# Optimization experiments

Hardware: AMD Instinct MI355X
Metric: run time of the kernel (lower is better)

The kernel has to match this reference:

```python
import jax, jax.numpy as jnp
import numpy as np

MARGIN = 0.5


def _pairwise_dist(x):
    # Euclidean cdist via ||a||^2 + ||b||^2 - 2ab, with safe sqrt.
    sq = jnp.sum(x * x, axis=-1)  # (N,)
    d2 = sq[:, None] + sq[None, :] - 2.0 * (x @ x.T)
    d2 = jnp.maximum(d2, 0.0)
    return jnp.sqrt(jnp.where(d2 > 0.0, d2, 1.0)) * (d2 > 0.0)


def setup_inputs() -> dict:
    key = jax.random.key(0)
    k1, k2 = jax.random.split(key)
    N, D = 8192, 128
    embeddings = jax.random.normal(k1, (N, D), dtype=jnp.float32)
    labels = jax.random.randint(k2, (N,), 0, 7, dtype=jnp.int64)
    return {"embeddings": embeddings, "labels": labels}


def reference(embeddings, labels):
    N = embeddings.shape[0]
    dist = _pairwise_dist(embeddings)  # (N, N)
    same = labels[:, None] == labels[None, :]
    eye = jnp.eye(N, dtype=bool)
    pos_mask = same & ~eye
    neg_mask = ~same
    big = jnp.asarray(jnp.finfo(dist.dtype).max, dist.dtype)
    # hardest positive: max dist among same-label (excl. self)
    pos_dist = jnp.max(jnp.where(pos_mask, dist, -big), axis=1)
    # hardest negative: min dist among different-label
    neg_dist = jnp.min(jnp.where(neg_mask, dist, big), axis=1)
    valid = jnp.any(pos_mask, axis=1) & jnp.any(neg_mask, axis=1)
    per_row = jax.nn.relu(pos_dist - neg_dist + MARGIN)
    loss_sum = jnp.sum(jnp.where(valid, per_row, 0.0))
    count = jnp.sum(valid)
    return loss_sum / jnp.maximum(count, 1).astype(loss_sum.dtype)
```

## Files before the change

### kernel.cpp

```cpp
#include <hip/hip_runtime.h>

#define N 8192
#define D 128
#define MARGIN 0.5f
#define FLT_BIG 3.402823466e+38f

typedef __bf16 bf16x8 __attribute__((ext_vector_type(8)));
typedef float f32x4 __attribute__((ext_vector_type(4)));
typedef unsigned short u16x8 __attribute__((ext_vector_type(8)));

__device__ __forceinline__ unsigned short f2bf_rne(float f) {
  unsigned u = __float_as_uint(f);
  u += 0x7FFFu + ((u >> 16) & 1u);
  return (unsigned short)(u >> 16);
}

#define FRAG_OFF(tile, k, lane) ((size_t)(tile) * 2048 + (size_t)(k) * 512 + (size_t)(lane) * 8)

__global__ void k_prep(const float* __restrict__ x, const int* __restrict__ lab,
                       unsigned short* __restrict__ xb, float* __restrict__ sq,
                       unsigned* __restrict__ posw, unsigned* __restrict__ negw,
                       unsigned* __restrict__ hist, float* __restrict__ acc,
                       unsigned* __restrict__ ticket) {
  const int t = threadIdx.x;
  const int row = blockIdx.x * 16 + (t >> 4);
  const int c = t & 15;
  const float4 v0 = ((const float4*)x)[row * 32 + c * 2];
  const float4 v1 = ((const float4*)x)[row * 32 + c * 2 + 1];
  u16x8 o;
  o[0] = f2bf_rne(v0.x); o[1] = f2bf_rne(v0.y);
  o[2] = f2bf_rne(v0.z); o[3] = f2bf_rne(v0.w);
  o[4] = f2bf_rne(v1.x); o[5] = f2bf_rne(v1.y);
  o[6] = f2bf_rne(v1.z); o[7] = f2bf_rne(v1.w);
  *(u16x8*)(xb + FRAG_OFF(row >> 4, c >> 2, ((c & 3) * 16) + (row & 15))) = o;
  float s = v0.x * v0.x + v0.y * v0.y + v0.z * v0.z + v0.w * v0.w +
            v1.x * v1.x + v1.y * v1.y + v1.z * v1.z + v1.w * v1.w;
#pragma unroll
  for (int off = 1; off < 16; off <<= 1) s += __shfl_xor(s, off, 64);
  if (c == 0) {
    sq[row] = s;
    posw[row] = 0u;
    negw[row] = 0x7F800000u;
  }

  if (blockIdx.x == 0) {
    __shared__ unsigned h[8];
    if (t < 8) h[t] = 0u;
    __syncthreads();
    unsigned long long cA = 0ull, cB = 0ull;
#pragma unroll
    for (int it = 0; it < 32; ++it) {
      const int l = lab[t + it * 256] & 7;
      if (l < 4) cA += 1ull << (l * 16);
      else       cB += 1ull << ((l - 4) * 16);
    }
#pragma unroll
    for (int off = 1; off < 64; off <<= 1) {
      cA += __shfl_xor(cA, off, 64);
      cB += __shfl_xor(cB, off, 64);
    }
    if ((t & 63) == 0) {
#pragma unroll
      for (int q = 0; q < 4; ++q) {
        atomicAdd(&h[q],     (unsigned)((cA >> (q * 16)) & 0xFFFFu));
        atomicAdd(&h[4 + q], (unsigned)((cB >> (q * 16)) & 0xFFFFu));
      }
    }
    __syncthreads();
    if (t < 8) hist[t] = h[t];
    if (t == 0) { acc[0] = 0.f; acc[1] = 0.f; ticket[0] = 0u; }
  }
}

__global__ __launch_bounds__(256, 3) void k_mine(
    const unsigned short* __restrict__ xb, const float* __restrict__ sq,
    const int* __restrict__ lab, unsigned* __restrict__ posw, unsigned* __restrict__ negw) {
  const int t = threadIdx.x;
  const int w = t >> 6;
  const int lane = t & 63;
  const int col = lane & 15;
  const int quad = lane >> 4;
  const int i0 = blockIdx.x * 256 + w * 64;
  const int jbase = blockIdx.y * 256;

  bf16x8 a[4][4];
#pragma unroll
  for (int is = 0; is < 4; ++is)
#pragma unroll
    for (int k = 0; k < 4; ++k)
      a[is][k] = *(const bf16x8*)(xb + FRAG_OFF((i0 >> 4) + is, k, lane));

  unsigned lab4[4];
#pragma unroll
  for (int is = 0; is < 4; ++is) {
    const int b = i0 + is * 16 + quad * 4;
    lab4[is] = (unsigned)(lab[b] & 255) | ((unsigned)(lab[b + 1] & 255) << 8) |
               ((unsigned)(lab[b + 2] & 255) << 16) | ((unsigned)(lab[b + 3] & 255) << 24);
  }

  float pos[4][4], neg[4][4];
#pragma unroll
  for (int is = 0; is < 4; ++is)
#pragma unroll
    for (int r = 0; r < 4; ++r) { pos[is][r] = -FLT_BIG; neg[is][r] = FLT_BIG; }

  const int jt0 = jbase >> 4;
  const float* sqp = sq + jbase + col;
  const int* labp = lab + jbase + col;

#pragma unroll 1
  for (int js = 0; js < 16; ++js) {
    const float sqj = sqp[js * 16];
    const unsigned labj = (unsigned)(labp[js * 16] & 255) * 0x01010101u;
    const unsigned short* g = xb + FRAG_OFF(jt0 + js, 0, lane);
    const bf16x8 b0 = *(const bf16x8*)(g);
    const bf16x8 b1 = *(const bf16x8*)(g + 512);
    const bf16x8 b2 = *(const bf16x8*)(g + 1024);
    const bf16x8 b3 = *(const bf16x8*)(g + 1536);

    f32x4 ac[4];
#pragma unroll
    for (int is = 0; is < 4; ++is) {
      ac[is] = (f32x4){0.f, 0.f, 0.f, 0.f};
      ac[is] = __builtin_amdgcn_mfma_f32_16x16x32_bf16(a[is][0], b0, ac[is], 0, 0, 0);
      ac[is] = __builtin_amdgcn_mfma_f32_16x16x32_bf16(a[is][1], b1, ac[is], 0, 0, 0);
      ac[is] = __builtin_amdgcn_mfma_f32_16x16x32_bf16(a[is][2], b2, ac[is], 0, 0, 0);
      ac[is] = __builtin_amdgcn_mfma_f32_16x16x32_bf16(a[is][3], b3, ac[is], 0, 0, 0);
    }

#pragma unroll
    for (int is = 0; is < 4; ++is) {
      const unsigned diff = lab4[is] ^ labj;
#pragma unroll
      for (int r = 0; r < 4; ++r) {
        const float m = fmaf(-2.f, ac[is][r], sqj);
        const bool same = ((diff >> (r * 8)) & 255u) == 0u;
        pos[is][r] = fmaxf(pos[is][r], same ? m : -FLT_BIG);
        neg[is][r] = fminf(neg[is][r], same ? FLT_BIG : m);
      }
    }
  }

#pragma unroll
  for (int is = 0; is < 4; ++is)
#pragma unroll
    for (int r = 0; r < 4; ++r) {
      float p = pos[is][r], n = neg[is][r];
#pragma unroll
      for (int off = 1; off < 16; off <<= 1) {
        p = fmaxf(p, __shfl_xor(p, off, 64));
        n = fminf(n, __shfl_xor(n, off, 64));
      }
      if (col == 0) {
        const int i = i0 + is * 16 + quad * 4 + r;
        const float sqi = sq[i];
        atomicMax(posw + i, __float_as_uint(fmaxf(sqi + p, 0.f)));
        atomicMin(negw + i, __float_as_uint(fmaxf(sqi + n, 0.f)));
      }
    }
}

__global__ void k_tail(const unsigned* __restrict__ posw, const unsigned* __restrict__ negw,
                       const int* __restrict__ lab, const unsigned* __restrict__ hist,
                       float* __restrict__ acc, unsigned* __restrict__ ticket,
                       float* __restrict__ out) {
  __shared__ float ls[4], cs[4];
  const int t = threadIdx.x;
  const int i = blockIdx.x * 256 + t;
  const float pd2 = __uint_as_float(posw[i]);
  const float nd2 = __uint_as_float(negw[i]);
  const unsigned cnt = hist[lab[i] & 7];
  const bool valid = (cnt >= 2u) && (cnt < (unsigned)N);
  float loss = 0.f, c = 0.f;
  if (valid) {
    loss = fmaxf(sqrtf(pd2) - sqrtf(fminf(nd2, FLT_BIG)) + MARGIN, 0.f);
    c = 1.f;
  }
#pragma unroll
  for (int off = 1; off < 64; off <<= 1) {
    loss += __shfl_xor(loss, off, 64);
    c += __shfl_xor(c, off, 64);
  }
  const int wv = t >> 6;
  if ((t & 63) == 0) { ls[wv] = loss; cs[wv] = c; }
  __syncthreads();
  if (t == 0) {
    atomicAdd(acc + 0, ls[0] + ls[1] + ls[2] + ls[3]);
    atomicAdd(acc + 1, cs[0] + cs[1] + cs[2] + cs[3]);
    __threadfence();
    const unsigned tk = atomicAdd(ticket, 1u);
    if (tk == 31u) {
      const float lsum = atomicAdd(acc + 0, 0.f);
      const float csum = atomicAdd(acc + 1, 0.f);
      out[0] = lsum / fmaxf(csum, 1.f);
    }
  }
}

extern "C" void kernel_launch(void* const* d_in, const int* in_sizes, int n_in,
                              void* d_out, int out_size, void* d_ws, size_t ws_size,
                              hipStream_t stream) {
  const float* x = (const float*)d_in[0];
  const int* lab = (const int*)d_in[1];
  char* ws = (char*)d_ws;
  unsigned short* xb = (unsigned short*)ws;
  float* sq = (float*)(ws + (size_t)N * D * 2);
  unsigned* posw = (unsigned*)((char*)sq + (size_t)N * 4);
  unsigned* negw = posw + N;
  unsigned* hist = negw + N;
  unsigned* ticket = hist + 8;
  float* acc = (float*)(ticket + 1);
  float* out = (float*)d_out;

  hipLaunchKernelGGL(k_prep, dim3(512), dim3(256), 0, stream, x, lab, xb, sq,
                     posw, negw, hist, acc, ticket);
  hipLaunchKernelGGL(k_mine, dim3(32, 32), dim3(256), 0, stream, xb, sq, lab, posw, negw);
  hipLaunchKernelGGL(k_tail, dim3(32), dim3(256), 0, stream, posw, negw, lab, hist,
                     acc, ticket, out);
}
```

Before: 110.2 us.

## Sort rows by label and specialize uniform-label tiles in mining loop

Adds a single-block histogram and prefix-scan kernel so rows can be scattered into label-sorted order. The bf16 fragments, squared norms and labels are all written in that permuted order. In the mining loop, 16x16 tiles whose row and column groups share one label only update the positive max, and tiles with disjoint label ranges only update the negative min, skipping the per-element compare and select. This adds an extra serial one-block launch and a scatter. Label ties within a tile are still handled by the generic path.

```diff
diff --git a/kernel.cpp b/kernel.cpp
--- a/kernel.cpp
+++ b/kernel.cpp
@@ -17,14 +17,86 @@
 
 #define FRAG_OFF(tile, k, lane) ((size_t)(tile) * 2048 + (size_t)(k) * 512 + (size_t)(lane) * 8)
 
+__global__ void k_hist(const int* __restrict__ lab, unsigned* __restrict__ chunkbase,
+                       unsigned* __restrict__ cnt8, float* __restrict__ acc,
+                       unsigned* __restrict__ ticket) {
+  __shared__ unsigned short cnt[512][8];
+  __shared__ unsigned exc[512][8];
+  __shared__ unsigned total[8], labbase[8];
+  const int t = threadIdx.x;
+  const int lane = t & 63;
+  const int w = t >> 6;
+
+#pragma unroll
+  for (int cc = 0; cc < 2; ++cc) {
+    const int c = t * 2 + cc;
+    unsigned long long cA = 0ull, cB = 0ull;
+#pragma unroll
+    for (int r = 0; r < 16; ++r) {
+      const int l = lab[c * 16 + r] & 7;
+      if (l < 4) cA += 1ull << (l * 16);
+      else       cB += 1ull << ((l - 4) * 16);
+    }
+#pragma unroll
+    for (int g = 0; g < 4; ++g) {
+      cnt[c][g]     = (unsigned short)((cA >> (g * 16)) & 0xFFFFu);
+      cnt[c][4 + g] = (unsigned short)((cB >> (g * 16)) & 0xFFFFu);
+    }
+  }
+  __syncthreads();
+
+  for (int g = w; g < 8; g += 4) {
+    unsigned run = 0;
+    for (int blk = 0; blk < 8; ++blk) {
+      const unsigned v = cnt[blk * 64 + lane][g];
+      unsigned x = v;
+#pragma unroll
+      for (int off = 1; off < 64; off <<= 1) {
+        const unsigned y = __shfl_up(x, off, 64);
+        if (lane >= off) x += y;
+      }
+      exc[blk * 64 + lane][g] = run + x - v;
+      run += __builtin_amdgcn_readlane(x, 63);
+    }
+    if (lane == 0) total[g] = run;
+  }
+  __syncthreads();
+  if (t == 0) {
+    unsigned run = 0;
+#pragma unroll
+    for (int g = 0; g < 8; ++g) { labbase[g] = run; run += total[g]; cnt8[g] = total[g]; }
+    acc[0] = 0.f; acc[1] = 0.f; ticket[0] = 0u;
+  }
+  __syncthreads();
+#pragma unroll
+  for (int e = 0; e < 16; ++e) {
+    const int idx = t * 16 + e;
+    chunkbase[idx] = labbase[idx & 7] + exc[idx >> 3][idx & 7];
+  }
+}
+
 __global__ void k_prep(const float* __restrict__ x, const int* __restrict__ lab,
+                       const unsigned* __restrict__ chunkbase,
                        unsigned short* __restrict__ xb, float* __restrict__ sq,
-                       unsigned* __restrict__ posw, unsigned* __restrict__ negw,
-                       unsigned* __restrict__ hist, float* __restrict__ acc,
-                       unsigned* __restrict__ ticket) {
-  const int t = threadIdx.x;
-  const int row = blockIdx.x * 16 + (t >> 4);
+                       int* __restrict__ lab_s, unsigned* __restrict__ posw,
+                       unsigned* __restrict__ negw) {
+  __shared__ int lab16[16];
+  __shared__ unsigned p16[16];
+  const int t = threadIdx.x;
+  const int rl = t >> 4;
   const int c = t & 15;
+  const int row = blockIdx.x * 16 + rl;
+  if (c == 0) lab16[rl] = lab[row] & 7;
+  __syncthreads();
+  if (t < 16) {
+    const int lg = lab16[t];
+    int rank = 0;
+    for (int r2 = 0; r2 < t; ++r2) rank += (lab16[r2] == lg) ? 1 : 0;
+    p16[t] = chunkbase[blockIdx.x * 8 + lg] + rank;
+  }
+  __syncthreads();
+  const unsigned p = p16[rl];
+
   const float4 v0 = ((const float4*)x)[row * 32 + c * 2];
   const float4 v1 = ((const float4*)x)[row * 32 + c * 2 + 1];
   u16x8 o;
@@ -32,49 +104,22 @@
   o[2] = f2bf_rne(v0.z); o[3] = f2bf_rne(v0.w);
   o[4] = f2bf_rne(v1.x); o[5] = f2bf_rne(v1.y);
   o[6] = f2bf_rne(v1.z); o[7] = f2bf_rne(v1.w);
-  *(u16x8*)(xb + FRAG_OFF(row >> 4, c >> 2, ((c & 3) * 16) + (row & 15))) = o;
+  *(u16x8*)(xb + FRAG_OFF(p >> 4, c >> 2, ((c & 3) * 16) + (int)(p & 15))) = o;
   float s = v0.x * v0.x + v0.y * v0.y + v0.z * v0.z + v0.w * v0.w +
             v1.x * v1.x + v1.y * v1.y + v1.z * v1.z + v1.w * v1.w;
 #pragma unroll
   for (int off = 1; off < 16; off <<= 1) s += __shfl_xor(s, off, 64);
   if (c == 0) {
-    sq[row] = s;
-    posw[row] = 0u;
-    negw[row] = 0x7F800000u;
-  }
-
-  if (blockIdx.x == 0) {
-    __shared__ unsigned h[8];
-    if (t < 8) h[t] = 0u;
-    __syncthreads();
-    unsigned long long cA = 0ull, cB = 0ull;
-#pragma unroll
-    for (int it = 0; it < 32; ++it) {
-      const int l = lab[t + it * 256] & 7;
-      if (l < 4) cA += 1ull << (l * 16);
-      else       cB += 1ull << ((l - 4) * 16);
-    }
-#pragma unroll
-    for (int off = 1; off < 64; off <<= 1) {
-      cA += __shfl_xor(cA, off, 64);
-      cB += __shfl_xor(cB, off, 64);
-    }
-    if ((t & 63) == 0) {
-#pragma unroll
-      for (int q = 0; q < 4; ++q) {
-        atomicAdd(&h[q],     (unsigned)((cA >> (q * 16)) & 0xFFFFu));
-        atomicAdd(&h[4 + q], (unsigned)((cB >> (q * 16)) & 0xFFFFu));
-      }
-    }
-    __syncthreads();
-    if (t < 8) hist[t] = h[t];
-    if (t == 0) { acc[0] = 0.f; acc[1] = 0.f; ticket[0] = 0u; }
+    sq[p] = s;
+    lab_s[p] = lab16[rl];
+    posw[p] = 0u;
+    negw[p] = 0x7F800000u;
   }
 }
 
 __global__ __launch_bounds__(256, 3) void k_mine(
     const unsigned short* __restrict__ xb, const float* __restrict__ sq,
-    const int* __restrict__ lab, unsigned* __restrict__ posw, unsigned* __restrict__ negw) {
+    const int* __restrict__ lab_s, unsigned* __restrict__ posw, unsigned* __restrict__ negw) {
   const int t = threadIdx.x;
   const int w = t >> 6;
   const int lane = t & 63;
@@ -90,12 +135,18 @@
     for (int k = 0; k < 4; ++k)
       a[is][k] = *(const bf16x8*)(xb + FRAG_OFF((i0 >> 4) + is, k, lane));
 
+  int gilo[4], gihi[4];
+#pragma unroll
+  for (int is = 0; is < 4; ++is) {
+    gilo[is] = __builtin_amdgcn_readfirstlane(lab_s[i0 + is * 16]);
+    gihi[is] = __builtin_amdgcn_readfirstlane(lab_s[i0 + is * 16 + 15]);
+  }
   unsigned lab4[4];
 #pragma unroll
   for (int is = 0; is < 4; ++is) {
     const int b = i0 + is * 16 + quad * 4;
-    lab4[is] = (unsigned)(lab[b] & 255) | ((unsigned)(lab[b + 1] & 255) << 8) |
-               ((unsigned)(lab[b + 2] & 255) << 16) | ((unsigned)(lab[b + 3] & 255) << 24);
+    lab4[is] = (unsigned)(lab_s[b] & 255) | ((unsigned)(lab_s[b + 1] & 255) << 8) |
+               ((unsigned)(lab_s[b + 2] & 255) << 16) | ((unsigned)(lab_s[b + 3] & 255) << 24);
   }
 
   float pos[4][4], neg[4][4];
@@ -106,12 +157,14 @@
 
   const int jt0 = jbase >> 4;
   const float* sqp = sq + jbase + col;
-  const int* labp = lab + jbase + col;
+  const int* labp = lab_s + jbase + col;
 
 #pragma unroll 1
   for (int js = 0; js < 16; ++js) {
     const float sqj = sqp[js * 16];
-    const unsigned labj = (unsigned)(labp[js * 16] & 255) * 0x01010101u;
+    const int labjv = labp[js * 16] & 7;
+    const int gjlo = __builtin_amdgcn_readfirstlane(labjv);
+    const int gjhi = __builtin_amdgcn_readlane(labjv, 15);
     const unsigned short* g = xb + FRAG_OFF(jt0 + js, 0, lane);
     const bf16x8 b0 = *(const bf16x8*)(g);
     const bf16x8 b1 = *(const bf16x8*)(g + 512);
@@ -130,13 +183,23 @@
 
 #pragma unroll
     for (int is = 0; is < 4; ++is) {
-      const unsigned diff = lab4[is] ^ labj;
-#pragma unroll
-      for (int r = 0; r < 4; ++r) {
-        const float m = fmaf(-2.f, ac[is][r], sqj);
-        const bool same = ((diff >> (r * 8)) & 255u) == 0u;
-        pos[is][r] = fmaxf(pos[is][r], same ? m : -FLT_BIG);
-        neg[is][r] = fminf(neg[is][r], same ? FLT_BIG : m);
+      if (gilo[is] == gihi[is] && gilo[is] == gjlo && gjlo == gjhi) {
+#pragma unroll
+        for (int r = 0; r < 4; ++r)
+          pos[is][r] = fmaxf(pos[is][r], fmaf(-2.f, ac[is][r], sqj));
+      } else if (gihi[is] < gjlo || gjhi < gilo[is]) {
+#pragma unroll
+        for (int r = 0; r < 4; ++r)
+          neg[is][r] = fminf(neg[is][r], fmaf(-2.f, ac[is][r], sqj));
+      } else {
+        const unsigned diff = lab4[is] ^ ((unsigned)labjv * 0x01010101u);
+#pragma unroll
+        for (int r = 0; r < 4; ++r) {
+          const float m = fmaf(-2.f, ac[is][r], sqj);
+          const bool same = ((diff >> (r * 8)) & 255u) == 0u;
+          pos[is][r] = fmaxf(pos[is][r], same ? m : -FLT_BIG);
+          neg[is][r] = fminf(neg[is][r], same ? FLT_BIG : m);
+        }
       }
     }
   }
@@ -161,7 +224,7 @@
 }
 
 __global__ void k_tail(const unsigned* __restrict__ posw, const unsigned* __restrict__ negw,
-                       const int* __restrict__ lab, const unsigned* __restrict__ hist,
+                       const int* __restrict__ lab_s, const unsigned* __restrict__ hist,
                        float* __restrict__ acc, unsigned* __restrict__ ticket,
                        float* __restrict__ out) {
   __shared__ float ls[4], cs[4];
@@ -169,7 +232,7 @@
   const int i = blockIdx.x * 256 + t;
   const float pd2 = __uint_as_float(posw[i]);
   const float nd2 = __uint_as_float(negw[i]);
-  const unsigned cnt = hist[lab[i] & 7];
+  const unsigned cnt = hist[lab_s[i] & 7];
   const bool valid = (cnt >= 2u) && (cnt < (unsigned)N);
   float loss = 0.f, c = 0.f;
   if (valid) {
@@ -207,14 +270,17 @@
   float* sq = (float*)(ws + (size_t)N * D * 2);
   unsigned* posw = (unsigned*)((char*)sq + (size_t)N * 4);
   unsigned* negw = posw + N;
-  unsigned* hist = negw + N;
+  int* lab_s = (int*)(negw + N);
+  unsigned* chunkbase = (unsigned*)(lab_s + N);
+  unsigned* hist = chunkbase + 512 * 8;
   unsigned* ticket = hist + 8;
   float* acc = (float*)(ticket + 1);
   float* out = (float*)d_out;
 
-  hipLaunchKernelGGL(k_prep, dim3(512), dim3(256), 0, stream, x, lab, xb, sq,
-                     posw, negw, hist, acc, ticket);
-  hipLaunchKernelGGL(k_mine, dim3(32, 32), dim3(256), 0, stream, xb, sq, lab, posw, negw);
-  hipLaunchKernelGGL(k_tail, dim3(32), dim3(256), 0, stream, posw, negw, lab, hist,
+  hipLaunchKernelGGL(k_hist, dim3(1), dim3(256), 0, stream, lab, chunkbase, hist, acc, ticket);
+  hipLaunchKernelGGL(k_prep, dim3(512), dim3(256), 0, stream, x, lab, chunkbase,
+                     xb, sq, lab_s, posw, negw);
+  hipLaunchKernelGGL(k_mine, dim3(32, 32), dim3(256), 0, stream, xb, sq, lab_s, posw, negw);
+  hipLaunchKernelGGL(k_tail, dim3(32), dim3(256), 0, stream, posw, negw, lab_s, hist,
                      acc, ticket, out);
 }
```

Result: slower. 127.2 us (+15.4%).
